# Optimization experiments

Measured on AMD Instinct MI355X. Metric: run time of the kernel, lower is better.

## Reference

```python
import jax, jax.numpy as jnp
import numpy as np

B, H, P, D = 4, 16, 1024, 128

def setup_inputs() -> dict:
    key = jax.random.key(0)
    kq, kk = jax.random.split(key)
    q = jax.random.normal(kq, (B, H, P, D), dtype=jnp.float32)
    k = jax.random.normal(kk, (B, H, P, D), dtype=jnp.float32)
    scale = jnp.full((1,), 1.0 / np.sqrt(D), dtype=jnp.float32)
    return {"q": q, "k": k, "scale": scale}

def reference(q, k, scale):
    # base_fun (SiLU) applied as the basis nonlinearity on q and k,
    # then patch-wise attention scores scaled by `scale`, softmax over keys.
    qb = jax.nn.silu(q)  # [B,H,P,D]
    kb = jax.nn.silu(k)  # [B,H,P,D]
    scores = jnp.einsum('bhpd,bhqd->bhpq', qb, kb) * scale  # [B,H,P,P]
    return jax.nn.softmax(scores, axis=-1)
```

## Files before the change

kernel.cpp:

```cpp
#include <hip/hip_runtime.h>
#include <stdint.h>
#include <stddef.h>

#define BHC 64
#define PP  1024
#define DD  128
#define BM  64
#define BN  128
#define NCH 8
#define LSTR 136

typedef __bf16 bf16x8 __attribute__((ext_vector_type(8)));
typedef float  f32x4  __attribute__((ext_vector_type(4)));

__device__ __forceinline__ unsigned short f2bf(float x) {
    union { float f; uint32_t u; } v; v.f = x;
    uint32_t r = v.u + 0x7FFFu + ((v.u >> 16) & 1u);
    return (unsigned short)(r >> 16);
}

__global__ void silu_cast_kernel(const float* __restrict__ q, const float* __restrict__ k,
                                 unsigned short* __restrict__ qb, unsigned short* __restrict__ kb,
                                 int n4each) {
    int stride = gridDim.x * blockDim.x;
    int total  = 2 * n4each;
    for (int i = blockIdx.x * blockDim.x + threadIdx.x; i < total; i += stride) {
        const float4* s; ushort4* d; int j;
        if (i < n4each) { s = (const float4*)q; d = (ushort4*)qb; j = i; }
        else            { s = (const float4*)k; d = (ushort4*)kb; j = i - n4each; }
        float4 x = s[j];
        float4 y;
        y.x = x.x / (1.f + __expf(-x.x));
        y.y = x.y / (1.f + __expf(-x.y));
        y.z = x.z / (1.f + __expf(-x.z));
        y.w = x.w / (1.f + __expf(-x.w));
        ushort4 o;
        o.x = f2bf(y.x); o.y = f2bf(y.y); o.z = f2bf(y.z); o.w = f2bf(y.w);
        d[j] = o;
    }
}

__global__ __launch_bounds__(1024) void attn_kernel(
        const unsigned short* __restrict__ qb, const unsigned short* __restrict__ kb,
        const float* __restrict__ scale, float* __restrict__ out) {
    __shared__ unsigned short qs [BM * LSTR];
    __shared__ unsigned short ksm[BN * LSTR];
    __shared__ float red_m[BM * 8];
    __shared__ float red_l[BM * 8];

    int bx   = blockIdx.x;
    int xcd  = bx & 7;
    int idx  = bx >> 3;
    int bh   = xcd * 8 + (idx >> 4);
    int qblk = idx & 15;

    int t    = threadIdx.x;
    int lane = t & 63;
    int w    = t >> 6;
    int wr   = w & 1;
    int wc   = w >> 1;
    int l15  = lane & 15;
    int quad = lane >> 4;

    const unsigned short* qg = qb + (size_t)bh * (PP * DD) + (size_t)qblk * (BM * DD);
    const unsigned short* kg = kb + (size_t)bh * (PP * DD);

    {
        int row = t >> 4, u = t & 15;
        uint4 v = *(const uint4*)(qg + row * DD + u * 8);
        *(uint4*)(&qs[row * LSTR + u * 8]) = v;
    }
    __syncthreads();

    bf16x8 aF[2][4];
#pragma unroll
    for (int rt = 0; rt < 2; ++rt)
#pragma unroll
        for (int kk = 0; kk < 4; ++kk)
            aF[rt][kk] = *(const bf16x8*)(&qs[(wr * 32 + rt * 16 + l15) * LSTR + kk * 32 + quad * 8]);

    f32x4 acc[NCH][2];
#pragma unroll
    for (int c = 0; c < NCH; ++c) {
        acc[c][0] = (f32x4)0.0f;
        acc[c][1] = (f32x4)0.0f;
    }

#pragma unroll
    for (int c = 0; c < NCH; ++c) {
        __syncthreads();
        {
            int u0 = t,        r0 = u0 >> 4, c0 = u0 & 15;
            int u1 = t + 1024, r1 = u1 >> 4, c1 = u1 & 15;
            uint4 v0 = *(const uint4*)(kg + (c * BN + r0) * DD + c0 * 8);
            uint4 v1 = *(const uint4*)(kg + (c * BN + r1) * DD + c1 * 8);
            *(uint4*)(&ksm[r0 * LSTR + c0 * 8]) = v0;
            *(uint4*)(&ksm[r1 * LSTR + c1 * 8]) = v1;
        }
        __syncthreads();
#pragma unroll
        for (int kk = 0; kk < 4; ++kk) {
            bf16x8 bF = *(const bf16x8*)(&ksm[(wc * 16 + l15) * LSTR + kk * 32 + quad * 8]);
            acc[c][0] = __builtin_amdgcn_mfma_f32_16x16x32_bf16(aF[0][kk], bF, acc[c][0], 0, 0, 0);
            acc[c][1] = __builtin_amdgcn_mfma_f32_16x16x32_bf16(aF[1][kk], bF, acc[c][1], 0, 0, 0);
        }
    }

    float C2 = scale[0] * 1.44269504088896340736f;

#pragma unroll
    for (int rt = 0; rt < 2; ++rt) {
#pragma unroll
        for (int r = 0; r < 4; ++r) {
            float m = acc[0][rt][r];
#pragma unroll
            for (int c = 1; c < NCH; ++c) m = fmaxf(m, acc[c][rt][r]);
#pragma unroll
            for (int off = 1; off < 16; off <<= 1) m = fmaxf(m, __shfl_xor(m, off, 64));
            if (l15 == 0) red_m[(wr * 32 + rt * 16 + quad * 4 + r) * 8 + wc] = m;
        }
    }
    __syncthreads();

#pragma unroll
    for (int rt = 0; rt < 2; ++rt) {
#pragma unroll
        for (int r = 0; r < 4; ++r) {
            int row = wr * 32 + rt * 16 + quad * 4 + r;
            float4 p0 = *(const float4*)(&red_m[row * 8]);
            float4 p1 = *(const float4*)(&red_m[row * 8 + 4]);
            float m = fmaxf(fmaxf(fmaxf(p0.x, p0.y), fmaxf(p0.z, p0.w)),
                            fmaxf(fmaxf(p1.x, p1.y), fmaxf(p1.z, p1.w)));
            float ssum = 0.f;
#pragma unroll
            for (int c = 0; c < NCH; ++c) {
                float e = exp2f((acc[c][rt][r] - m) * C2);
                acc[c][rt][r] = e;
                ssum += e;
            }
#pragma unroll
            for (int off = 1; off < 16; off <<= 1) ssum += __shfl_xor(ssum, off, 64);
            if (l15 == 0) red_l[row * 8 + wc] = ssum;
        }
    }
    __syncthreads();

    float inv[2][4];
#pragma unroll
    for (int rt = 0; rt < 2; ++rt) {
#pragma unroll
        for (int r = 0; r < 4; ++r) {
            int row = wr * 32 + rt * 16 + quad * 4 + r;
            float4 p0 = *(const float4*)(&red_l[row * 8]);
            float4 p1 = *(const float4*)(&red_l[row * 8 + 4]);
            float l = (p0.x + p0.y) + (p0.z + p0.w) + (p1.x + p1.y) + (p1.z + p1.w);
            inv[rt][r] = 1.0f / l;
        }
    }

    float* og = out + ((size_t)bh << 20) + (size_t)(qblk * BM) * PP;
#pragma unroll
    for (int c = 0; c < NCH; ++c) {
#pragma unroll
        for (int rt = 0; rt < 2; ++rt) {
            int key = c * BN + wc * 16 + l15;
            int rb  = wr * 32 + rt * 16 + quad * 4;
#pragma unroll
            for (int r = 0; r < 4; ++r) {
                og[(size_t)(rb + r) * PP + key] = acc[c][rt][r] * inv[rt][r];
            }
        }
    }
}

extern "C" void kernel_launch(void* const* d_in, const int* in_sizes, int n_in,
                              void* d_out, int out_size, void* d_ws, size_t ws_size,
                              hipStream_t stream) {
    const float* q     = (const float*)d_in[0];
    const float* k     = (const float*)d_in[1];
    const float* scale = (const float*)d_in[2];
    float* out = (float*)d_out;

    unsigned short* qb = (unsigned short*)d_ws;
    unsigned short* kb = qb + (size_t)BHC * PP * DD;

    int n4each = (BHC * PP * DD) / 4;
    silu_cast_kernel<<<2048, 256, 0, stream>>>(q, k, qb, kb, n4each);
    attn_kernel<<<1024, 1024, 0, stream>>>(qb, kb, scale, out);
}
```

Measured before the change: 377.9 us.

## Fuse SiLU and bf16 cast into attention kernel with register-prefetched K tiles

Removes the separate SiLU/cast pre-pass and its bf16 workspace round trip. The attention kernel now reads fp32 q and k directly, applies SiLU and converts to bf16 while staging tiles into shared memory. The next K chunk is loaded into registers while the current chunk's MFMAs run. In exchange, SiLU on K is recomputed by each of the 16 query blocks per head, and each block reads twice the bytes of fp32 K.

```diff
diff --git a/kernel.cpp b/kernel.cpp
--- a/kernel.cpp
+++ b/kernel.cpp
@@ -19,29 +19,21 @@
     return (unsigned short)(r >> 16);
 }
 
-__global__ void silu_cast_kernel(const float* __restrict__ q, const float* __restrict__ k,
-                                 unsigned short* __restrict__ qb, unsigned short* __restrict__ kb,
-                                 int n4each) {
-    int stride = gridDim.x * blockDim.x;
-    int total  = 2 * n4each;
-    for (int i = blockIdx.x * blockDim.x + threadIdx.x; i < total; i += stride) {
-        const float4* s; ushort4* d; int j;
-        if (i < n4each) { s = (const float4*)q; d = (ushort4*)qb; j = i; }
-        else            { s = (const float4*)k; d = (ushort4*)kb; j = i - n4each; }
-        float4 x = s[j];
-        float4 y;
-        y.x = x.x / (1.f + __expf(-x.x));
-        y.y = x.y / (1.f + __expf(-x.y));
-        y.z = x.z / (1.f + __expf(-x.z));
-        y.w = x.w / (1.f + __expf(-x.w));
-        ushort4 o;
-        o.x = f2bf(y.x); o.y = f2bf(y.y); o.z = f2bf(y.z); o.w = f2bf(y.w);
-        d[j] = o;
-    }
+__device__ __forceinline__ float silu_f(float x) {
+    return x / (1.f + __expf(-x));
+}
+
+__device__ __forceinline__ uint4 pack8(const float4 a, const float4 b) {
+    uint4 o;
+    o.x = (uint32_t)f2bf(silu_f(a.x)) | ((uint32_t)f2bf(silu_f(a.y)) << 16);
+    o.y = (uint32_t)f2bf(silu_f(a.z)) | ((uint32_t)f2bf(silu_f(a.w)) << 16);
+    o.z = (uint32_t)f2bf(silu_f(b.x)) | ((uint32_t)f2bf(silu_f(b.y)) << 16);
+    o.w = (uint32_t)f2bf(silu_f(b.z)) | ((uint32_t)f2bf(silu_f(b.w)) << 16);
+    return o;
 }
 
 __global__ __launch_bounds__(1024) void attn_kernel(
-        const unsigned short* __restrict__ qb, const unsigned short* __restrict__ kb,
+        const float* __restrict__ q, const float* __restrict__ k,
         const float* __restrict__ scale, float* __restrict__ out) {
     __shared__ unsigned short qs [BM * LSTR];
     __shared__ unsigned short ksm[BN * LSTR];
@@ -62,14 +54,28 @@
     int l15  = lane & 15;
     int quad = lane >> 4;
 
-    const unsigned short* qg = qb + (size_t)bh * (PP * DD) + (size_t)qblk * (BM * DD);
-    const unsigned short* kg = kb + (size_t)bh * (PP * DD);
+    const float* qg = q + (size_t)bh * (PP * DD) + (size_t)qblk * (BM * DD);
+    const float* kg = k + (size_t)bh * (PP * DD);
 
     {
         int row = t >> 4, u = t & 15;
-        uint4 v = *(const uint4*)(qg + row * DD + u * 8);
-        *(uint4*)(&qs[row * LSTR + u * 8]) = v;
+        const float* p = qg + row * DD + u * 8;
+        float4 a = *(const float4*)p;
+        float4 b = *(const float4*)(p + 4);
+        *(uint4*)(&qs[row * LSTR + u * 8]) = pack8(a, b);
     }
+
+    int r0  = t >> 4;
+    int r1  = r0 + 64;
+    int cu  = t & 15;
+    float4 f0a, f0b, f1a, f1b;
+    {
+        const float* p0 = kg + (size_t)(r0) * DD + cu * 8;
+        const float* p1 = kg + (size_t)(r1) * DD + cu * 8;
+        f0a = *(const float4*)p0; f0b = *(const float4*)(p0 + 4);
+        f1a = *(const float4*)p1; f1b = *(const float4*)(p1 + 4);
+    }
+
     __syncthreads();
 
     bf16x8 aF[2][4];
@@ -88,16 +94,18 @@
 
 #pragma unroll
     for (int c = 0; c < NCH; ++c) {
+        uint4 pk0 = pack8(f0a, f0b);
+        uint4 pk1 = pack8(f1a, f1b);
         __syncthreads();
-        {
-            int u0 = t,        r0 = u0 >> 4, c0 = u0 & 15;
-            int u1 = t + 1024, r1 = u1 >> 4, c1 = u1 & 15;
-            uint4 v0 = *(const uint4*)(kg + (c * BN + r0) * DD + c0 * 8);
-            uint4 v1 = *(const uint4*)(kg + (c * BN + r1) * DD + c1 * 8);
-            *(uint4*)(&ksm[r0 * LSTR + c0 * 8]) = v0;
-            *(uint4*)(&ksm[r1 * LSTR + c1 * 8]) = v1;
+        *(uint4*)(&ksm[r0 * LSTR + cu * 8]) = pk0;
+        *(uint4*)(&ksm[r1 * LSTR + cu * 8]) = pk1;
+        __syncthreads();
+        if (c < NCH - 1) {
+            const float* p0 = kg + (size_t)((c + 1) * BN + r0) * DD + cu * 8;
+            const float* p1 = kg + (size_t)((c + 1) * BN + r1) * DD + cu * 8;
+            f0a = *(const float4*)p0; f0b = *(const float4*)(p0 + 4);
+            f1a = *(const float4*)p1; f1b = *(const float4*)(p1 + 4);
         }
-        __syncthreads();
 #pragma unroll
         for (int kk = 0; kk < 4; ++kk) {
             bf16x8 bF = *(const bf16x8*)(&ksm[(wc * 16 + l15) * LSTR + kk * 32 + quad * 8]);
@@ -180,11 +188,7 @@
     const float* k     = (const float*)d_in[1];
     const float* scale = (const float*)d_in[2];
     float* out = (float*)d_out;
+    (void)d_ws; (void)ws_size;
 
-    unsigned short* qb = (unsigned short*)d_ws;
-    unsigned short* kb = qb + (size_t)BHC * PP * DD;
-
-    int n4each = (BHC * PP * DD) / 4;
-    silu_cast_kernel<<<2048, 256, 0, stream>>>(q, k, qb, kb, n4each);
-    attn_kernel<<<1024, 1024, 0, stream>>>(qb, kb, scale, out);
+    attn_kernel<<<1024, 1024, 0, stream>>>(q, k, scale, out);
 }
```

Result: slower. 424.2 us (+12.2%).

## Load MFMA operands directly from global memory with register prefetch, drop LDS staging

Applied to the files above, without the earlier changes.

The attention kernel no longer stages Q and K tiles through shared memory with barriers. Each wave loads its bf16 MFMA fragments straight from global (L2-resident) memory and prefetches the next key chunk into registers while computing the current one. The intent is to remove the LDS round trips and the per-chunk __syncthreads. The trade-off is redundant global loads across waves sharing a K tile and less coalesced access patterns. The SiLU kernel also switches from a division to a fast reciprocal.

```diff
diff --git a/kernel.cpp b/kernel.cpp
--- a/kernel.cpp
+++ b/kernel.cpp
@@ -8,7 +8,6 @@
 #define BM  64
 #define BN  128
 #define NCH 8
-#define LSTR 136
 
 typedef __bf16 bf16x8 __attribute__((ext_vector_type(8)));
 typedef float  f32x4  __attribute__((ext_vector_type(4)));
@@ -17,6 +16,10 @@
     union { float f; uint32_t u; } v; v.f = x;
     uint32_t r = v.u + 0x7FFFu + ((v.u >> 16) & 1u);
     return (unsigned short)(r >> 16);
+}
+
+__device__ __forceinline__ float silu_f(float x) {
+    return x * __builtin_amdgcn_rcpf(1.f + __expf(-x));
 }
 
 __global__ void silu_cast_kernel(const float* __restrict__ q, const float* __restrict__ k,
@@ -29,13 +32,9 @@
         if (i < n4each) { s = (const float4*)q; d = (ushort4*)qb; j = i; }
         else            { s = (const float4*)k; d = (ushort4*)kb; j = i - n4each; }
         float4 x = s[j];
-        float4 y;
-        y.x = x.x / (1.f + __expf(-x.x));
-        y.y = x.y / (1.f + __expf(-x.y));
-        y.z = x.z / (1.f + __expf(-x.z));
-        y.w = x.w / (1.f + __expf(-x.w));
         ushort4 o;
-        o.x = f2bf(y.x); o.y = f2bf(y.y); o.z = f2bf(y.z); o.w = f2bf(y.w);
+        o.x = f2bf(silu_f(x.x)); o.y = f2bf(silu_f(x.y));
+        o.z = f2bf(silu_f(x.z)); o.w = f2bf(silu_f(x.w));
         d[j] = o;
     }
 }
@@ -43,8 +42,6 @@
 __global__ __launch_bounds__(1024) void attn_kernel(
         const unsigned short* __restrict__ qb, const unsigned short* __restrict__ kb,
         const float* __restrict__ scale, float* __restrict__ out) {
-    __shared__ unsigned short qs [BM * LSTR];
-    __shared__ unsigned short ksm[BN * LSTR];
     __shared__ float red_m[BM * 8];
     __shared__ float red_l[BM * 8];
 
@@ -65,19 +62,12 @@
     const unsigned short* qg = qb + (size_t)bh * (PP * DD) + (size_t)qblk * (BM * DD);
     const unsigned short* kg = kb + (size_t)bh * (PP * DD);
 
-    {
-        int row = t >> 4, u = t & 15;
-        uint4 v = *(const uint4*)(qg + row * DD + u * 8);
-        *(uint4*)(&qs[row * LSTR + u * 8]) = v;
-    }
-    __syncthreads();
-
     bf16x8 aF[2][4];
 #pragma unroll
     for (int rt = 0; rt < 2; ++rt)
 #pragma unroll
         for (int kk = 0; kk < 4; ++kk)
-            aF[rt][kk] = *(const bf16x8*)(&qs[(wr * 32 + rt * 16 + l15) * LSTR + kk * 32 + quad * 8]);
+            aF[rt][kk] = *(const bf16x8*)(qg + (wr * 32 + rt * 16 + l15) * DD + kk * 32 + quad * 8);
 
     f32x4 acc[NCH][2];
 #pragma unroll
@@ -86,24 +76,26 @@
         acc[c][1] = (f32x4)0.0f;
     }
 
+    const unsigned short* kl = kg + (wc * 16 + l15) * DD + quad * 8;
+    bf16x8 bF[4], bN[4];
+#pragma unroll
+    for (int kk = 0; kk < 4; ++kk)
+        bF[kk] = *(const bf16x8*)(kl + kk * 32);
+
 #pragma unroll
     for (int c = 0; c < NCH; ++c) {
-        __syncthreads();
-        {
-            int u0 = t,        r0 = u0 >> 4, c0 = u0 & 15;
-            int u1 = t + 1024, r1 = u1 >> 4, c1 = u1 & 15;
-            uint4 v0 = *(const uint4*)(kg + (c * BN + r0) * DD + c0 * 8);
-            uint4 v1 = *(const uint4*)(kg + (c * BN + r1) * DD + c1 * 8);
-            *(uint4*)(&ksm[r0 * LSTR + c0 * 8]) = v0;
-            *(uint4*)(&ksm[r1 * LSTR + c1 * 8]) = v1;
+        if (c < NCH - 1) {
+#pragma unroll
+            for (int kk = 0; kk < 4; ++kk)
+                bN[kk] = *(const bf16x8*)(kl + (size_t)(c + 1) * (BN * DD) + kk * 32);
         }
-        __syncthreads();
 #pragma unroll
         for (int kk = 0; kk < 4; ++kk) {
-            bf16x8 bF = *(const bf16x8*)(&ksm[(wc * 16 + l15) * LSTR + kk * 32 + quad * 8]);
-            acc[c][0] = __builtin_amdgcn_mfma_f32_16x16x32_bf16(aF[0][kk], bF, acc[c][0], 0, 0, 0);
-            acc[c][1] = __builtin_amdgcn_mfma_f32_16x16x32_bf16(aF[1][kk], bF, acc[c][1], 0, 0, 0);
+            acc[c][0] = __builtin_amdgcn_mfma_f32_16x16x32_bf16(aF[0][kk], bF[kk], acc[c][0], 0, 0, 0);
+            acc[c][1] = __builtin_amdgcn_mfma_f32_16x16x32_bf16(aF[1][kk], bF[kk], acc[c][1], 0, 0, 0);
         }
+#pragma unroll
+        for (int kk = 0; kk < 4; ++kk) bF[kk] = bN[kk];
     }
 
     float C2 = scale[0] * 1.44269504088896340736f;
```

After: 417.6 us. +10.5%, slower.
